# Kernel optimization log

Hardware: AMD Instinct MI355X
Metric: run time of the kernel (lower is better)

Reference implementation:

```python
import jax, jax.numpy as jnp
import numpy as np
from jax import lax

K = 32            # module k
T = 1             # train_ensemble -> times_sampled
LARGE = 1e10      # LARGE_NUMBER in source
NEG = -1e30       # finite stand-in for -inf (keeps grads NaN-free)


def prefix_logesp(theta, k):
    """Prefix log elementary symmetric polynomials of weights w_i = exp(theta_i).
    theta: (BE, N). Returns F of shape (N+1, BE, k+1) with F[i, b, j] = log e_j(w_1..w_i).
    """
    BE = theta.shape[0]
    init = jnp.concatenate([jnp.zeros((BE, 1), theta.dtype),
                            jnp.full((BE, k), NEG, theta.dtype)], axis=1)

    def step(E, th):
        shifted = jnp.concatenate([jnp.full((BE, 1), NEG, E.dtype), E[:, :-1]], axis=1) + th[:, None]
        Enew = jnp.logaddexp(E, shifted)
        return Enew, Enew

    _, Es = lax.scan(step, init, theta.T)            # Es: (N, BE, k+1)
    return jnp.concatenate([init[None], Es], axis=0)  # (N+1, BE, k+1)


def simple_core(flat, k, times_sampled, key):
    """SIMPLE k-subset layer: exact marginals (log_pr) + conditional-Poisson sampling,
    with straight-through gradient through the marginals (matches the .detach() trick).
    flat: (BE, N) logits. Returns samples (T, BE, N) and marginals (BE, N).
    """
    BE, N = flat.shape
    F = prefix_logesp(flat, k)                       # prefix ESPs, (N+1, BE, k+1)
    B = prefix_logesp(flat[:, ::-1], k)[::-1]        # suffix ESPs: B[i] = ESP of items i..N-1

    # marginal p_i = w_i * e_{k-1}(w \ i) / e_k(w)
    comb = F[:N, :, :k] + B[1:, :, :k][:, :, ::-1]   # (N, BE, k): j + (k-1-j) split
    log_ekm1 = jax.scipy.special.logsumexp(comb, axis=2)  # (N, BE)
    logZ = F[N, :, k]                                # (BE,) log e_k of all weights
    logp = flat.T + log_ekm1 - logZ[None]            # (N, BE)
    marginals = jnp.exp(logp).T                      # (BE, N)

    # exact sequential sampling from the k-subset (conditional Poisson) distribution
    U = jax.random.uniform(key, (N, times_sampled, BE))
    be = jnp.arange(BE)[None, :]

    def samp_step(r, xs):
        th_i, Bi, Bip1, u = xs                       # th_i: (BE,), Bi/Bip1: (BE, k+1), u: (T, BE)
        rm1 = jnp.maximum(r - 1, 0)
        logq = th_i[None, :] + Bip1[be, rm1] - Bi[be, r]
        incl = (u < jnp.exp(jnp.minimum(logq, 0.0))) & (r > 0)
        return r - incl.astype(r.dtype), incl.astype(flat.dtype)

    r0 = jnp.full((times_sampled, BE), k, dtype=jnp.int32)
    _, bits = lax.scan(samp_step, r0, (flat.T, B[:-1], B[1:], U))  # bits: (N, T, BE)
    samples = jnp.transpose(bits, (1, 2, 0))         # (T, BE, N) hard k-hot
    # straight-through: (samples - marginals).detach() + marginals
    samples = lax.stop_gradient(samples - marginals[None]) + marginals[None]
    return samples, marginals


def setup_inputs() -> dict:
    key = jax.random.key(0)
    scores = jax.random.normal(key, (128, 4096, 2), dtype=jnp.float32)
    return {"scores": scores}


def reference(scores):
    bsz, Nmax, ens = scores.shape
    # policy == 'edge_candid'
    flat = jnp.transpose(scores, (0, 2, 1)).reshape(bsz * ens, Nmax)
    target = Nmax
    k = min(K, Nmax)
    N = 2 ** int(np.ceil(np.log2(target)))
    if N > target:  # pad to power of 2 with -LARGE (no-op for Nmax=4096)
        pad = jnp.full((flat.shape[0], N - target), -LARGE, flat.dtype)
        flat = jnp.concatenate([flat, pad], axis=1)
    # logits_activation is None -> pass through
    samples, marginals = simple_core(flat, k, T, jax.random.key(42))
    samples = samples[..., :target]
    marginals = marginals[:, :target]
    new_mask = samples.reshape(T, bsz, ens, Nmax).transpose(0, 1, 3, 2)      # (T, B, Nmax, E)
    new_marginals = marginals.reshape(bsz, ens, Nmax).transpose(0, 2, 1)     # (B, Nmax, E)
    return new_mask, new_marginals
```

## Files before the change

kernel.cpp:

```cpp
#include <hip/hip_runtime.h>
#include <stdint.h>

#pragma clang fp contract(off)

#define BE_C     256
#define N_C      4096
#define K_C      32
#define NEG_C    (-1e30f)
#define OUT_HALF 1048576

__device__ __forceinline__ float xla_exp_neg(float x) {
  const float exp_lo = -88.3762626647949f;
  const float log2ef = 1.44269504088896341f;
  const float c1 = 0.693359375f;
  const float c2 = -2.12194440e-4f;
  const float p0 = 1.9875691500E-4f;
  const float p1 = 1.3981999507E-3f;
  const float p2 = 8.3334519073E-3f;
  const float p3 = 4.1665795894E-2f;
  const float p4 = 1.6666665459E-1f;
  const float p5 = 5.0000001201E-1f;
  float xc = fmaxf(x, exp_lo);
  float fx = floorf(xc * log2ef + 0.5f);
  float tmp = c1 * fx;
  float z = c2 * fx;
  float xx = xc - tmp;
  xx = xx - z;
  z = xx * xx;
  float y = xx * p0 + p1;
  y = y * xx + p2;
  y = y * xx + p3;
  y = y * xx + p4;
  y = y * xx + p5;
  y = y * z + xx;
  y = y + 1.0f;
  int ei = (int)fx;
  float s = __int_as_float((ei + 127) << 23);
  return y * s;
}

__device__ __forceinline__ float xla_log_12(float xin) {
  const float sqrthf = 0.707106781186547524f;
  const float p0 = 7.0376836292E-2f;
  const float p1 = -1.1514610310E-1f;
  const float p2 = 1.1676998740E-1f;
  const float p3 = -1.2420140846E-1f;
  const float p4 = 1.4249322787E-1f;
  const float p5 = -1.6668057665E-1f;
  const float p6 = 2.0000714765E-1f;
  const float p7 = -2.4999993993E-1f;
  const float p8 = 3.3333331174E-1f;
  const float q1 = -2.12194440e-4f;
  const float q2 = 0.693359375f;
  float x = xin;
  unsigned ub = __float_as_uint(x);
  int emm0 = (int)(ub >> 23) - 0x7f;
  float e = 1.0f + (float)emm0;
  x = __uint_as_float((ub & 0x007fffffu) | 0x3f000000u);
  bool mlt = x < sqrthf;
  float tmp = mlt ? x : 0.0f;
  x = x - 1.0f;
  e = e - (mlt ? 1.0f : 0.0f);
  x = x + tmp;
  float x2 = x * x;
  float x3 = x2 * x;
  float y  = x * p0 + p1;
  float y1 = x * p3 + p4;
  float y2 = x * p6 + p7;
  y  = y * x + p2;
  y1 = y1 * x + p5;
  y2 = y2 * x + p8;
  y = y * x3 + y1;
  y = y * x3 + y2;
  y = y * x3;
  y1 = q1 * e;
  float t2 = 0.5f * x2;
  y = y + y1;
  x = x - t2;
  y2 = q2 * e;
  x = x + y;
  x = x + y2;
  return x;
}

__device__ __forceinline__ float xla_log1p_01(float x) {
  float fsmall = ((-0.5f * x) + 1.0f) * x;
  float flarge = xla_log_12(x + 1.0f);
  return (fabsf(x) < 1e-4f) ? fsmall : flarge;
}

__device__ __forceinline__ float xla_logaddexp(float a, float b) {
  float mx = fmaxf(a, b);
  float d = a - b;
  float e = xla_exp_neg(-fabsf(d));
  return mx + xla_log1p_01(e);
}

__device__ __forceinline__ float fast_la(float a, float b) {
  float mx = fmaxf(a, b);
  float d = a - b;
  float e = __expf(-fabsf(d));
  return mx + __logf(1.0f + e);
}

__device__ __forceinline__ float dpp_shr1(float x, float fill) {
  int r = __builtin_amdgcn_update_dpp(__float_as_int(fill), __float_as_int(x),
                                      0x138, 0xF, 0xF, false);
  return __int_as_float(r);
}

__device__ __forceinline__ float readlane_f(float v, int l) {
  return __int_as_float(__builtin_amdgcn_readlane(__float_as_int(v), l));
}

__device__ __forceinline__ unsigned rotl_(unsigned v, int r) {
  return (v << r) | (v >> (32 - r));
}

__device__ __forceinline__ void threefry_0_42(unsigned c0, unsigned c1,
                                              unsigned* o0, unsigned* o1) {
  const unsigned ks0 = 0u, ks1 = 42u, ks2 = 0x1BD11BDAu ^ 0u ^ 42u;
  unsigned x0 = c0 + ks0, x1 = c1 + ks1;
  x0 += x1; x1 = rotl_(x1, 13); x1 ^= x0;
  x0 += x1; x1 = rotl_(x1, 15); x1 ^= x0;
  x0 += x1; x1 = rotl_(x1, 26); x1 ^= x0;
  x0 += x1; x1 = rotl_(x1, 6);  x1 ^= x0;
  x0 += ks1; x1 += ks2 + 1u;
  x0 += x1; x1 = rotl_(x1, 17); x1 ^= x0;
  x0 += x1; x1 = rotl_(x1, 29); x1 ^= x0;
  x0 += x1; x1 = rotl_(x1, 16); x1 ^= x0;
  x0 += x1; x1 = rotl_(x1, 24); x1 ^= x0;
  x0 += ks2; x1 += ks0 + 2u;
  x0 += x1; x1 = rotl_(x1, 13); x1 ^= x0;
  x0 += x1; x1 = rotl_(x1, 15); x1 ^= x0;
  x0 += x1; x1 = rotl_(x1, 26); x1 ^= x0;
  x0 += x1; x1 = rotl_(x1, 6);  x1 ^= x0;
  x0 += ks0; x1 += ks1 + 3u;
  x0 += x1; x1 = rotl_(x1, 17); x1 ^= x0;
  x0 += x1; x1 = rotl_(x1, 29); x1 ^= x0;
  x0 += x1; x1 = rotl_(x1, 16); x1 ^= x0;
  x0 += x1; x1 = rotl_(x1, 24); x1 ^= x0;
  x0 += ks1; x1 += ks2 + 4u;
  x0 += x1; x1 = rotl_(x1, 13); x1 ^= x0;
  x0 += x1; x1 = rotl_(x1, 15); x1 ^= x0;
  x0 += x1; x1 = rotl_(x1, 26); x1 ^= x0;
  x0 += x1; x1 = rotl_(x1, 6);  x1 ^= x0;
  x0 += ks2; x1 += ks0 + 5u;
  *o0 = x0; *o1 = x1;
}

__device__ __forceinline__ float u01_from_idx(unsigned idx) {
  unsigned b0, b1;
  threefry_0_42(0u, idx, &b0, &b1);
  unsigned bits = b0 ^ b1;
  unsigned fb = (bits >> 9) | 0x3f800000u;
  return __uint_as_float(fb) - 1.0f;
}

__device__ __forceinline__ int sw_idx(int row, int col) {
  return row * 32 + ((col + row) & 31);
}

__global__ __launch_bounds__(256)
void EdgeSIMPLEBatched_39298950758997_kernel(const float* __restrict__ scores,
                                             float* __restrict__ out) {
  __shared__ float th_lds[N_C];
  __shared__ float chkB[64 * 32];
  __shared__ float chkF[63 * 32];
  __shared__ float logZ_s;
  __shared__ union OvT {
    float u[N_C];
    float wbuf[4][64 * 32];
  } ov;

  const int t = threadIdx.x;
  const int w = t >> 6;
  const int lane = t & 63;
  const int b = blockIdx.x;
  const int bi = b >> 1, ens = b & 1;
  const float* srow = scores + bi * (N_C * 2) + ens;
  const int obase = bi * (N_C * 2) + ens;

  for (int idx = t; idx < N_C; idx += 256) {
    th_lds[idx] = srow[idx * 2];
    ov.u[idx] = u01_from_idx((unsigned)(idx * BE_C + b));
  }
  __syncthreads();

  if (w == 0) {
    float E = (lane == 0) ? 0.0f : NEG_C;
    if (lane < 32) chkB[63 * 32 + lane] = E;
    const int l31 = lane & 31;
    float thb = th_lds[N_C - 1 - l31];
    float ub  = ov.u[N_C - 1 - l31];
    unsigned Wbits = 0u;
#pragma unroll 1
    for (int g = 0; g < 128; ++g) {
      const int nb = (g + 1 < 128) ? g + 1 : g;
      float thb_n = th_lds[N_C - 1 - nb * 32 - l31];
      float ub_n  = ov.u[N_C - 1 - nb * 32 - l31];
#pragma unroll 4
      for (int l = 0; l < 32; ++l) {
        float th = readlane_f(thb, l);
        float u  = readlane_f(ub, l);
        float Em1 = dpp_shr1(E, NEG_C);
        float sh = Em1 + th;
        float Enew = xla_logaddexp(E, sh);
        float logq = (th + Em1) - Enew;
        float q = xla_exp_neg(fminf(logq, 0.0f));
        unsigned pb = (u < q) ? 1u : 0u;
        Wbits |= pb << l;
        E = Enew;
      }
      if (lane >= 1 && lane <= 32)
        out[obase + ((127 - g) * 32 + lane - 1) * 2] = __uint_as_float(Wbits);
      Wbits = 0u;
      if ((g & 1) == 1 && g < 127 && lane < 32)
        chkB[(((127 - g) >> 1) - 1) * 32 + lane] = E;
      thb = thb_n; ub = ub_n;
    }
    if (lane == 32) logZ_s = E;
  } else if (w == 1) {
    float F = (lane == 0) ? 0.0f : NEG_C;
    float th = th_lds[0];
#pragma unroll 2
    for (int i = 0; i < N_C; ++i) {
      float th_nx = th_lds[(i + 1 < N_C) ? i + 1 : i];
      if ((i & 63) == 0 && i > 0 && lane < 32) chkF[((i >> 6) - 1) * 32 + lane] = F;
      float Fm1 = dpp_shr1(F, NEG_C);
      F = fast_la(F, Fm1 + th);
      th = th_nx;
    }
  }
  __syncthreads();

  const float logZ = logZ_s;
  float* wb = ov.wbuf[w];
  for (int c = w; c < 64; c += 4) {
    float E2 = chkB[c * 32 + (lane & 31)];
    if (lane < 32) wb[sw_idx(63, lane)] = E2;
#pragma unroll 1
    for (int ii = 63; ii >= 1; --ii) {
      float th = th_lds[c * 64 + ii];
      float Em1 = dpp_shr1(E2, NEG_C);
      E2 = fast_la(E2, Em1 + th);
      if (lane < 32) wb[sw_idx(ii - 1, lane)] = E2;
    }
    float F2;
    if (c == 0) F2 = (lane == 0) ? 0.0f : NEG_C;
    else        F2 = (lane < 32) ? chkF[(c - 1) * 32 + lane] : NEG_C;
    float th = th_lds[c * 64];
#pragma unroll 2
    for (int ii = 0; ii < 64; ++ii) {
      float th_nx = th_lds[c * 64 + ((ii + 1 < 64) ? ii + 1 : ii)];
      float bbv = wb[sw_idx(ii, (31 - lane) & 31)];
      float comb = F2 + bbv;
      if (lane < 32) wb[sw_idx(ii, lane)] = comb;
      float Fm1 = dpp_shr1(F2, NEG_C);
      F2 = fast_la(F2, Fm1 + th);
      th = th_nx;
    }
    __threadfence_block();
    float cb[32];
#pragma unroll
    for (int jj = 0; jj < 32; ++jj) cb[jj] = wb[sw_idx(lane, jj)];
    float amax = cb[0];
#pragma unroll
    for (int jj = 1; jj < 32; ++jj) amax = fmaxf(amax, cb[jj]);
    float ss = 0.0f;
#pragma unroll
    for (int jj = 0; jj < 32; ++jj) ss += __expf(cb[jj] - amax);
    float thi = th_lds[c * 64 + lane];
    float m = __expf((thi + (__logf(ss) + amax)) - logZ);
    out[OUT_HALF + obase + (c * 64 + lane) * 2] = m;
  }
  __syncthreads();

  if (w == 0) {
    int r = K_C;
    const int l31 = lane & 31;
    unsigned Wv = 0u;
    if (lane >= 1 && lane <= 32)
      Wv = __float_as_uint(out[obase + (lane - 1) * 2]);
#pragma unroll 1
    for (int g = 127; g >= 0; --g) {
      unsigned Wn = 0u;
      if (g > 0 && lane >= 1 && lane <= 32)
        Wn = __float_as_uint(out[obase + ((128 - g) * 32 + lane - 1) * 2]);
      const int i_l = N_C - 1 - 32 * g - l31;
      float mval = out[OUT_HALF + obase + i_l * 2];
      unsigned inclW = 0u;
#pragma unroll 8
      for (int l = 31; l >= 0; --l) {
        unsigned mm = (unsigned)__builtin_amdgcn_readlane((int)Wv, r);
        unsigned bit = (mm >> l) & 1u;
        inclW |= bit << l;
        r -= (int)bit;
      }
      if (lane < 32) {
        unsigned incl = (inclW >> l31) & 1u;
        float sval = incl ? ((1.0f - mval) + mval) : 0.0f;
        out[obase + i_l * 2] = sval;
      }
      Wv = Wn;
    }
  }
}

extern "C" void kernel_launch(void* const* d_in, const int* in_sizes, int n_in,
                              void* d_out, int out_size, void* d_ws, size_t ws_size,
                              hipStream_t stream) {
  (void)in_sizes; (void)n_in; (void)d_ws; (void)ws_size; (void)out_size;
  const float* scores = (const float*)d_in[0];
  float* out = (float*)d_out;
  EdgeSIMPLEBatched_39298950758997_kernel<<<dim3(BE_C), dim3(256), 0, stream>>>(scores, out);
}
```

Baseline: 1.216 ms.

## Overlap per-chunk marginal computation with prefix/suffix scans via LDS flags and work claiming

Instead of waiting on a block barrier until both serial scans finish, waves claim 64-item chunks through an atomic counter and spin on LDS ready flags until the needed backward and forward checkpoints exist. This lets the marginal work run alongside the long sequential scans. Because logZ is not known until the backward scan ends, marginals are stored unnormalised and normalised in a separate pass. Uniform random numbers are now generated inline inside the backward scan rather than precomputed into LDS, which adds hash work to the serial critical path. The scan waves (0 and 1) also join the work queue once they finish.

```diff
diff --git a/kernel.cpp b/kernel.cpp
--- a/kernel.cpp
+++ b/kernel.cpp
@@ -167,11 +167,11 @@
   __shared__ float th_lds[N_C];
   __shared__ float chkB[64 * 32];
   __shared__ float chkF[63 * 32];
+  __shared__ float wbuf[4][64 * 32];
   __shared__ float logZ_s;
-  __shared__ union OvT {
-    float u[N_C];
-    float wbuf[4][64 * 32];
-  } ov;
+  __shared__ int   bReady;
+  __shared__ int   fReady;
+  __shared__ int   claimIdx;
 
   const int t = threadIdx.x;
   const int w = t >> 6;
@@ -180,25 +180,25 @@
   const int bi = b >> 1, ens = b & 1;
   const float* srow = scores + bi * (N_C * 2) + ens;
   const int obase = bi * (N_C * 2) + ens;
-
-  for (int idx = t; idx < N_C; idx += 256) {
-    th_lds[idx] = srow[idx * 2];
-    ov.u[idx] = u01_from_idx((unsigned)(idx * BE_C + b));
-  }
+  const int l31 = lane & 31;
+
+  for (int idx = t; idx < N_C; idx += 256) th_lds[idx] = srow[idx * 2];
+  if (t == 0) { bReady = 64; fReady = 0; claimIdx = 0; }
   __syncthreads();
 
   if (w == 0) {
     float E = (lane == 0) ? 0.0f : NEG_C;
     if (lane < 32) chkB[63 * 32 + lane] = E;
-    const int l31 = lane & 31;
+    __threadfence_block();
+    if (lane == 0) *(volatile int*)&bReady = 63;
     float thb = th_lds[N_C - 1 - l31];
-    float ub  = ov.u[N_C - 1 - l31];
+    float ub  = u01_from_idx((unsigned)((N_C - 1 - l31) * BE_C + b));
     unsigned Wbits = 0u;
 #pragma unroll 1
     for (int g = 0; g < 128; ++g) {
       const int nb = (g + 1 < 128) ? g + 1 : g;
       float thb_n = th_lds[N_C - 1 - nb * 32 - l31];
-      float ub_n  = ov.u[N_C - 1 - nb * 32 - l31];
+      float ub_n  = u01_from_idx((unsigned)((N_C - 1 - nb * 32 - l31) * BE_C + b));
 #pragma unroll 4
       for (int l = 0; l < 32; ++l) {
         float th = readlane_f(thb, l);
@@ -215,70 +215,95 @@
       if (lane >= 1 && lane <= 32)
         out[obase + ((127 - g) * 32 + lane - 1) * 2] = __uint_as_float(Wbits);
       Wbits = 0u;
-      if ((g & 1) == 1 && g < 127 && lane < 32)
-        chkB[(((127 - g) >> 1) - 1) * 32 + lane] = E;
+      if ((g & 1) == 1 && g < 127) {
+        const int c = ((127 - g) >> 1) - 1;
+        if (lane < 32) chkB[c * 32 + lane] = E;
+        __threadfence_block();
+        if (lane == 0) *(volatile int*)&bReady = c;
+      }
       thb = thb_n; ub = ub_n;
     }
     if (lane == 32) logZ_s = E;
+    __threadfence_block();
+    if (lane == 0) *(volatile int*)&bReady = 0;
   } else if (w == 1) {
     float F = (lane == 0) ? 0.0f : NEG_C;
     float th = th_lds[0];
 #pragma unroll 2
     for (int i = 0; i < N_C; ++i) {
       float th_nx = th_lds[(i + 1 < N_C) ? i + 1 : i];
-      if ((i & 63) == 0 && i > 0 && lane < 32) chkF[((i >> 6) - 1) * 32 + lane] = F;
+      if ((i & 63) == 0 && i > 0) {
+        if (lane < 32) chkF[((i >> 6) - 1) * 32 + lane] = F;
+        __threadfence_block();
+        if (lane == 0) *(volatile int*)&fReady = (i >> 6);
+      }
       float Fm1 = dpp_shr1(F, NEG_C);
       F = fast_la(F, Fm1 + th);
       th = th_nx;
     }
   }
-  __syncthreads();
-
-  const float logZ = logZ_s;
-  float* wb = ov.wbuf[w];
-  for (int c = w; c < 64; c += 4) {
-    float E2 = chkB[c * 32 + (lane & 31)];
-    if (lane < 32) wb[sw_idx(63, lane)] = E2;
+
+  {
+    float* wb = wbuf[w];
+    for (;;) {
+      int idxv = 0;
+      if (lane == 0) idxv = atomicAdd(&claimIdx, 1);
+      idxv = __shfl(idxv, 0);
+      if (idxv >= 64) break;
+      const int c = 63 - idxv;
+      while (*(volatile int*)&bReady > c) __builtin_amdgcn_s_sleep(2);
+      while (*(volatile int*)&fReady < c) __builtin_amdgcn_s_sleep(2);
+      float E2 = chkB[c * 32 + l31];
+      if (lane < 32) wb[sw_idx(63, lane)] = E2;
 #pragma unroll 1
-    for (int ii = 63; ii >= 1; --ii) {
-      float th = th_lds[c * 64 + ii];
-      float Em1 = dpp_shr1(E2, NEG_C);
-      E2 = fast_la(E2, Em1 + th);
-      if (lane < 32) wb[sw_idx(ii - 1, lane)] = E2;
-    }
-    float F2;
-    if (c == 0) F2 = (lane == 0) ? 0.0f : NEG_C;
-    else        F2 = (lane < 32) ? chkF[(c - 1) * 32 + lane] : NEG_C;
-    float th = th_lds[c * 64];
+      for (int ii = 63; ii >= 1; --ii) {
+        float th = th_lds[c * 64 + ii];
+        float Em1 = dpp_shr1(E2, NEG_C);
+        E2 = fast_la(E2, Em1 + th);
+        if (lane < 32) wb[sw_idx(ii - 1, lane)] = E2;
+      }
+      float F2;
+      if (c == 0) F2 = (lane == 0) ? 0.0f : NEG_C;
+      else        F2 = (lane < 32) ? chkF[(c - 1) * 32 + lane] : NEG_C;
+      float th = th_lds[c * 64];
 #pragma unroll 2
-    for (int ii = 0; ii < 64; ++ii) {
-      float th_nx = th_lds[c * 64 + ((ii + 1 < 64) ? ii + 1 : ii)];
-      float bbv = wb[sw_idx(ii, (31 - lane) & 31)];
-      float comb = F2 + bbv;
-      if (lane < 32) wb[sw_idx(ii, lane)] = comb;
-      float Fm1 = dpp_shr1(F2, NEG_C);
-      F2 = fast_la(F2, Fm1 + th);
-      th = th_nx;
-    }
-    __threadfence_block();
-    float cb[32];
+      for (int ii = 0; ii < 64; ++ii) {
+        float th_nx = th_lds[c * 64 + ((ii + 1 < 64) ? ii + 1 : ii)];
+        float bbv = wb[sw_idx(ii, (31 - lane) & 31)];
+        float comb = F2 + bbv;
+        if (lane < 32) wb[sw_idx(ii, lane)] = comb;
+        float Fm1 = dpp_shr1(F2, NEG_C);
+        F2 = fast_la(F2, Fm1 + th);
+        th = th_nx;
+      }
+      __threadfence_block();
+      float cb[32];
 #pragma unroll
-    for (int jj = 0; jj < 32; ++jj) cb[jj] = wb[sw_idx(lane, jj)];
-    float amax = cb[0];
+      for (int jj = 0; jj < 32; ++jj) cb[jj] = wb[sw_idx(lane, jj)];
+      float amax = cb[0];
 #pragma unroll
-    for (int jj = 1; jj < 32; ++jj) amax = fmaxf(amax, cb[jj]);
-    float ss = 0.0f;
+      for (int jj = 1; jj < 32; ++jj) amax = fmaxf(amax, cb[jj]);
+      float ss = 0.0f;
 #pragma unroll
-    for (int jj = 0; jj < 32; ++jj) ss += __expf(cb[jj] - amax);
-    float thi = th_lds[c * 64 + lane];
-    float m = __expf((thi + (__logf(ss) + amax)) - logZ);
-    out[OUT_HALF + obase + (c * 64 + lane) * 2] = m;
+      for (int jj = 0; jj < 32; ++jj) ss += __expf(cb[jj] - amax);
+      float thi = th_lds[c * 64 + lane];
+      float mraw = thi + (__logf(ss) + amax);
+      out[OUT_HALF + obase + (c * 64 + lane) * 2] = mraw;
+    }
   }
   __syncthreads();
 
+  {
+    const float logZ = logZ_s;
+    for (int idx = t; idx < N_C; idx += 256) {
+      const int o = OUT_HALF + obase + idx * 2;
+      out[o] = __expf(out[o] - logZ);
+    }
+  }
+  __syncthreads();
+
   if (w == 0) {
     int r = K_C;
-    const int l31 = lane & 31;
     unsigned Wv = 0u;
     if (lane >= 1 && lane <= 32)
       Wv = __float_as_uint(out[obase + (lane - 1) * 2]);
```

After: 1.019 ms. 1.19x faster.
